# Optimization experiments

Measured on AMD Instinct MI355X. Metric: run time of the kernel, lower is better.

Reference implementation:

```python
import jax, jax.numpy as jnp
import numpy as np

# Model constants (from init_kwargs)
NF, NC, E, B = 100000, 4000, 500000, 256
D_FACT, D_COMP = 1536, 27
HIDDEN, HEADS, CPH = 128, 4, 32  # out_per_head = hidden // heads
NUM_LAYERS = 2
TIME_DIM = 8
T_SCALE = 30.0
EDGE_DIM = 2 + TIME_DIM  # [sentiment, decay, time2vec]
ATTN_SCALE = 1.0  # 1 / attn_temperature
NEG_SLOPE = 0.2


def time_edge_features(ea, lam):
    # ea: [E, 2] = [sentiment, decay]; second column in [0,1] -> decay branch
    s = jnp.clip(ea[:, 0:1], -1.0, 1.0)
    decay = jnp.clip(ea[:, 1:2], 0.0, 1.0)
    lam = jnp.maximum(lam, 1e-6)
    delta_t = -jnp.log(jnp.maximum(decay, 1e-6)) / lam
    t = jnp.log1p(jnp.maximum(delta_t, 0.0)) / T_SCALE  # [E,1]
    freqs = jnp.arange(1, TIME_DIM, dtype=ea.dtype)      # [TIME_DIM-1]
    sins = jnp.sin(t * freqs)                            # [E,TIME_DIM-1]
    return jnp.concatenate([s, decay, sins, t], axis=-1)  # [E, EDGE_DIM]


def seg_softmax(logits, seg, n):
    # logits: [E,H]; softmax over edges sharing the same destination node
    m = jax.ops.segment_max(logits, seg, num_segments=n)
    z = jnp.exp(logits - m[seg])
    den = jax.ops.segment_sum(z, seg, num_segments=n)
    return z / (den[seg] + 1e-16)


def seg_mean(x, seg, n):
    s = jax.ops.segment_sum(x, seg, num_segments=n)
    cnt = jax.ops.segment_sum(jnp.ones((x.shape[0],), x.dtype), seg, num_segments=n)
    return s / jnp.maximum(cnt, 1.0)[:, None]


def layernorm(x, g, b, eps=1e-5):
    mu = jnp.mean(x, axis=-1, keepdims=True)
    var = jnp.var(x, axis=-1, keepdims=True)
    return (x - mu) * jax.lax.rsqrt(var + eps) * g + b


def setup_inputs() -> dict:
    key = jax.random.key(0)
    ks = jax.random.split(key, 32)

    x_fact = jax.random.normal(ks[0], (NF, D_FACT), jnp.float32)
    x_company = jax.random.normal(ks[1], (NC, D_COMP), jnp.float32)
    u = jax.random.uniform(ks[2], (E, 2), jnp.float32)
    edge_attr = jnp.concatenate([u[:, 0:1] * 2.0 - 1.0, u[:, 1:2]], axis=1)
    edge_index = jnp.stack([
        jax.random.randint(ks[3], (E,), 0, NF),
        jax.random.randint(ks[4], (E,), 0, NC),
    ]).astype(jnp.int32)
    batch_fact = jnp.sort(jax.random.randint(ks[5], (NF,), 0, B)).astype(jnp.int32)
    batch_company = jnp.sort(jax.random.randint(ks[6], (NC,), 0, B)).astype(jnp.int32)

    def p(k, shape):
        return jax.random.normal(k, shape, jnp.float32) * 0.05

    inp = dict(
        x_fact=x_fact, x_company=x_company, edge_attr=edge_attr,
        edge_index=edge_index, batch_fact=batch_fact, batch_company=batch_company,
        lambda_decay=jnp.array(0.01, jnp.float32),
        Wf=p(ks[7], (D_FACT, HIDDEN)), bf=jnp.zeros((HIDDEN,), jnp.float32),
        Wc=p(ks[8], (D_COMP, HIDDEN)), bc=jnp.zeros((HIDDEN,), jnp.float32),
        Wl=p(ks[9], (NUM_LAYERS, HIDDEN, HIDDEN)), bl=jnp.zeros((NUM_LAYERS, HIDDEN), jnp.float32),
        Wr=p(ks[10], (NUM_LAYERS, HIDDEN, HIDDEN)), br=jnp.zeros((NUM_LAYERS, HIDDEN), jnp.float32),
        We=p(ks[11], (NUM_LAYERS, EDGE_DIM, HIDDEN)), be=jnp.zeros((NUM_LAYERS, HIDDEN), jnp.float32),
        att=p(ks[12], (NUM_LAYERS, HEADS, CPH)),
        bias_out=jnp.zeros((NUM_LAYERS, HIDDEN), jnp.float32),
        ln_g=jnp.ones((NUM_LAYERS, HIDDEN), jnp.float32), ln_b=jnp.zeros((NUM_LAYERS, HIDDEN), jnp.float32),
        Wg=p(ks[13], (2 * HIDDEN, 1)), bg=jnp.zeros((1,), jnp.float32),
        W1=p(ks[14], (HIDDEN, HIDDEN)), b1=jnp.zeros((HIDDEN,), jnp.float32),
        W2=p(ks[15], (HIDDEN, 1)), b2=jnp.zeros((1,), jnp.float32),
    )
    return inp


def reference(x_fact, x_company, edge_attr, edge_index, batch_fact, batch_company,
              lambda_decay, Wf, bf, Wc, bc, Wl, bl, Wr, br, We, be, att, bias_out,
              ln_g, ln_b, Wg, bg, W1, b1, W2, b2):
    src, dst = edge_index[0], edge_index[1]
    ef = time_edge_features(edge_attr, lambda_decay)          # [E, EDGE_DIM]

    # per-node-type input encoders
    hf = jax.nn.relu(x_fact @ Wf + bf)                         # [NF, H]
    hc = jax.nn.relu(x_company @ Wc + bc)                      # [NC, H]
    n_c = x_company.shape[0]

    for l in range(NUM_LAYERS):
        # GATv2 (edge-conditioned, bipartite fact->company, share_weights=False)
        gl = (hf @ Wl[l] + bl[l]).reshape(-1, HEADS, CPH)      # src transform [NF,H,C]
        gr = (hc @ Wr[l] + br[l]).reshape(-1, HEADS, CPH)      # dst transform [NC,H,C]
        ge = (ef @ We[l] + be[l]).reshape(-1, HEADS, CPH)      # edge transform [E,H,C]
        e = jax.nn.leaky_relu(gl[src] + gr[dst] + ge, NEG_SLOPE)  # [E,H,C]
        logits = jnp.einsum('ehc,hc->eh', e, att[l]) * ATTN_SCALE  # [E,H]
        alpha = seg_softmax(logits, dst, n_c)                   # scatter-softmax over dst
        msg = alpha[..., None] * gl[src]                        # [E,H,C]
        out = jax.ops.segment_sum(msg, dst, num_segments=n_c).reshape(n_c, HIDDEN) + bias_out[l]
        hc = layernorm(hc + jax.nn.relu(out), ln_g[l], ln_b[l])  # residual + post-norm

    # gated readout over graphs in batch
    pf = seg_mean(hf, batch_fact, B)                            # [B,H]
    pc = seg_mean(hc, batch_company, B)                         # [B,H]
    g = jax.nn.sigmoid(jnp.concatenate([pf, pc], axis=-1) @ Wg + bg)  # [B,1]
    h = g * pf + (1.0 - g) * pc                                 # [B,H]
    logit = jax.nn.relu(h @ W1 + b1) @ W2 + b2                  # [B,1]
    return logit
```

## Files before the change

kernel.cpp:

```cpp
#include <hip/hip_runtime.h>
#include <hip/hip_bf16.h>
#include <hip/hip_fp16.h>
#include <math.h>

#define NFAC 100000
#define NCOMP 4000
#define NEDGE 500000
#define NB 256
#define DF 1536
#define DC 27
#define H 128
#define EDIM 10
#define EDIMP 16

typedef __attribute__((ext_vector_type(8))) short short8v;
typedef __attribute__((ext_vector_type(4))) float f32x4;

#define GLOAD_LDS16(g, l)                                                              \
  __builtin_amdgcn_global_load_lds((const __attribute__((address_space(1))) unsigned int*)(g), \
                                   (__attribute__((address_space(3))) unsigned int*)(l), 16, 0, 0)

__device__ __forceinline__ float group32_sum(float v) {
#pragma unroll
  for (int m = 16; m > 0; m >>= 1) v += __shfl_xor(v, m);
  return v;
}

__device__ __forceinline__ unsigned short bf16rn(float x) {
  unsigned int u = __float_as_uint(x);
  unsigned int r = (u + 0x7fffu + ((u >> 16) & 1u)) >> 16;
  return (unsigned short)r;
}
__device__ __forceinline__ float bf16tof(unsigned short h) {
  return __uint_as_float(((unsigned int)h) << 16);
}

__global__ void k_edge_feat(const float* __restrict__ ea, const float* __restrict__ lamp,
                            float* __restrict__ ef) {
  int e = blockIdx.x * blockDim.x + threadIdx.x;
  if (e >= NEDGE) return;
  float s   = fminf(fmaxf(ea[2 * e], -1.f), 1.f);
  float dec = fminf(fmaxf(ea[2 * e + 1], 0.f), 1.f);
  float lam = fmaxf(lamp[0], 1e-6f);
  float dt  = -logf(fmaxf(dec, 1e-6f)) / lam;
  float t   = log1pf(fmaxf(dt, 0.f)) * (1.f / 30.f);
  float* o = ef + (size_t)e * EDIMP;
  o[0] = s;
  o[1] = dec;
#pragma unroll
  for (int k = 1; k < 8; k++) o[1 + k] = __sinf(t * (float)k);
  o[9] = t;
  o[10] = 0.f; o[11] = 0.f; o[12] = 0.f; o[13] = 0.f; o[14] = 0.f; o[15] = 0.f;
}

__global__ void k_hist(const int* __restrict__ dst, int* __restrict__ deg) {
  int e = blockIdx.x * blockDim.x + threadIdx.x;
  if (e < NEDGE) atomicAdd(&deg[dst[e]], 1);
}

__global__ __launch_bounds__(1024) void k_scan(const int* __restrict__ deg, int* __restrict__ off) {
  __shared__ int s[4096];
  int t = threadIdx.x;
  for (int i = t; i < 4096; i += 1024) s[i] = (i < NCOMP) ? deg[i] : 0;
  __syncthreads();
  for (int d = 1; d < 4096; d <<= 1) {
    int vals[4];
#pragma unroll
    for (int j = 0; j < 4; j++) {
      int i = t + j * 1024;
      vals[j] = (i >= d) ? s[i - d] : 0;
    }
    __syncthreads();
#pragma unroll
    for (int j = 0; j < 4; j++) {
      int i = t + j * 1024;
      s[i] += vals[j];
    }
    __syncthreads();
  }
  for (int i = t; i < 4096; i += 1024) off[i + 1] = s[i];
  if (t == 0) off[0] = 0;
}

__global__ void k_scatter(const int* __restrict__ dst, const int* __restrict__ src,
                          const int* __restrict__ off, int* __restrict__ cur,
                          int* __restrict__ eid, int* __restrict__ srcs) {
  int e = blockIdx.x * blockDim.x + threadIdx.x;
  if (e < NEDGE) {
    int d = dst[e];
    int p = atomicAdd(&cur[d], 1);
    eid[off[d] + p] = e;
    srcs[off[d] + p] = src[e];
  }
}

__global__ void k_conv_w(const float* __restrict__ W, unsigned short* __restrict__ Bh,
                         unsigned short* __restrict__ Bl, int K) {
  int i = blockIdx.x * blockDim.x + threadIdx.x;
  if (i >= K * H) return;
  int k = i >> 7, c = i & 127;
  float x = W[i];
  unsigned short h = bf16rn(x);
  unsigned short l = bf16rn(x - bf16tof(h));
  Bh[(size_t)c * K + k] = h;
  Bl[(size_t)c * K + k] = l;
}

__global__ void k_conv_wl2(const float* __restrict__ Wl, unsigned short* __restrict__ Bh,
                           unsigned short* __restrict__ Bl) {
  int i = blockIdx.x * blockDim.x + threadIdx.x;
  if (i >= 2 * H * H) return;
  int l = i >> 14;
  int r = i & 16383;
  int k = r >> 7, c = r & 127;
  float x = Wl[i];
  unsigned short h = bf16rn(x);
  unsigned short lo = bf16rn(x - bf16tof(h));
  int col = c + 128 * l;
  Bh[(size_t)col * H + k] = h;
  Bl[(size_t)col * H + k] = lo;
}

__device__ __forceinline__ unsigned int packhi(unsigned int u1, unsigned int u0) {
  return __builtin_amdgcn_perm(u1, u0, 0x07060302u);
}

__device__ __forceinline__ void split8(const float4& a0, const float4& a1, short8v& ah,
                                       short8v& al) {
  float xs[8] = {a0.x, a0.y, a0.z, a0.w, a1.x, a1.y, a1.z, a1.w};
  unsigned int hu[8], lu[8];
#pragma unroll
  for (int j = 0; j < 8; j++) {
    unsigned int u = __float_as_uint(xs[j]);
    hu[j] = u & 0xffff0000u;
    lu[j] = __float_as_uint(xs[j] - __uint_as_float(hu[j]));
  }
  unsigned int hw[4], lw[4];
#pragma unroll
  for (int j = 0; j < 4; j++) {
    hw[j] = packhi(hu[2 * j + 1], hu[2 * j]);
    lw[j] = packhi(lu[2 * j + 1], lu[2 * j]);
  }
  ah = *(short8v*)hw;
  al = *(short8v*)lw;
}

__global__ __launch_bounds__(256, 2) void k_gemm_mfma(const float* __restrict__ A,
                                                      const unsigned short* __restrict__ Bth,
                                                      const unsigned short* __restrict__ Btl,
                                                      const float* __restrict__ bias,
                                                      float* __restrict__ C, int M, int K,
                                                      int dorelu, float* __restrict__ Cpart) {
  __shared__ __align__(16) char smem[2][32768];
  int tid = threadIdx.x;
  int wave = tid >> 6, lane = tid & 63;
  int m0 = blockIdx.x * 128;
  int wm = (wave >> 1) * 64, wn = (wave & 1) * 64;
  int fr = lane & 15, fg = lane >> 4;
  int nsplit = gridDim.y;
  int Ks = K / nsplit;
  int kbeg = blockIdx.y * Ks;
  int nIter = Ks >> 5;

  f32x4 acc[4][4];
#pragma unroll
  for (int i = 0; i < 4; i++)
#pragma unroll
    for (int j = 0; j < 4; j++) acc[i][j] = (f32x4){0.f, 0.f, 0.f, 0.f};

  int a_row = (lane >> 3);
  int a_s = lane & 7;
  int b_col = (lane >> 2);
  int b_s = lane & 3;

  auto stage = [&](int buf, int k0) {
    char* base = smem[buf];
#pragma unroll
    for (int q = 0; q < 4; q++) {
      int j = wave + 4 * q;
      int row = j * 8 + a_row;
      int grow = m0 + row;
      if (grow >= M) grow = 0;
      const float* src = A + (size_t)grow * K + k0 + ((a_s ^ (row & 7)) << 2);
      GLOAD_LDS16(src, base + j * 1024);
    }
#pragma unroll
    for (int q = 0; q < 2; q++) {
      int j = wave + 4 * q;
      int col = j * 16 + b_col;
      int soff = k0 + ((b_s ^ (col & 3)) << 3);
      GLOAD_LDS16(Bth + (size_t)col * K + soff, base + 16384 + j * 1024);
      GLOAD_LDS16(Btl + (size_t)col * K + soff, base + 24576 + j * 1024);
    }
  };

  stage(0, kbeg);
  __syncthreads();

  for (int it = 0; it < nIter; ++it) {
    int cur = it & 1;
    if (it + 1 < nIter) stage(cur ^ 1, kbeg + ((it + 1) << 5));
    const char* cb = smem[cur];
    short8v ah[4], al[4];
#pragma unroll
    for (int mf = 0; mf < 4; mf++) {
      int r = wm + 16 * mf + fr;
      int s0 = (2 * fg) ^ (r & 7);
      int s1 = (2 * fg + 1) ^ (r & 7);
      float4 a0 = *(const float4*)(cb + r * 128 + s0 * 16);
      float4 a1 = *(const float4*)(cb + r * 128 + s1 * 16);
      split8(a0, a1, ah[mf], al[mf]);
    }
#pragma unroll
    for (int nf = 0; nf < 4; nf++) {
      int c = wn + 16 * nf + fr;
      int sb = fg ^ (c & 3);
      short8v bh = *(const short8v*)(cb + 16384 + c * 64 + sb * 16);
      short8v bl = *(const short8v*)(cb + 24576 + c * 64 + sb * 16);
#pragma unroll
      for (int mf = 0; mf < 4; mf++) {
        acc[mf][nf] = __builtin_amdgcn_mfma_f32_16x16x32_bf16(ah[mf], bh, acc[mf][nf], 0, 0, 0);
        acc[mf][nf] = __builtin_amdgcn_mfma_f32_16x16x32_bf16(ah[mf], bl, acc[mf][nf], 0, 0, 0);
        acc[mf][nf] = __builtin_amdgcn_mfma_f32_16x16x32_bf16(al[mf], bh, acc[mf][nf], 0, 0, 0);
      }
    }
    __syncthreads();
  }

  if (nsplit == 1) {
#pragma unroll
    for (int mf = 0; mf < 4; mf++) {
      int rbase = m0 + wm + 16 * mf + 4 * fg;
#pragma unroll
      for (int nf = 0; nf < 4; nf++) {
        int col = wn + 16 * nf + fr;
        float bv = bias[col];
#pragma unroll
        for (int j = 0; j < 4; j++) {
          int row = rbase + j;
          if (row < M) {
            float v = acc[mf][nf][j] + bv;
            if (dorelu) v = fmaxf(v, 0.f);
            C[(size_t)row * H + col] = v;
          }
        }
      }
    }
  } else {
    float* P = Cpart + (size_t)blockIdx.y * M * H;
#pragma unroll
    for (int mf = 0; mf < 4; mf++) {
      int rbase = m0 + wm + 16 * mf + 4 * fg;
#pragma unroll
      for (int nf = 0; nf < 4; nf++) {
        int col = wn + 16 * nf + fr;
#pragma unroll
        for (int j = 0; j < 4; j++) {
          int row = rbase + j;
          if (row < M) P[(size_t)row * H + col] = acc[mf][nf][j];
        }
      }
    }
  }
}

__global__ __launch_bounds__(256, 2) void k_gemm_n256(const float* __restrict__ A,
                                                      const unsigned short* __restrict__ Bth,
                                                      const unsigned short* __restrict__ Btl,
                                                      const float* __restrict__ bias,
                                                      __half* __restrict__ C, int M) {
  __shared__ __align__(16) char smem[2][40960];
  const int K = 128;
  int tid = threadIdx.x;
  int wave = tid >> 6, lane = tid & 63;
  int m0 = blockIdx.x * 64;
  int wn = wave * 64;
  int fr = lane & 15, fg = lane >> 4;

  f32x4 acc[4][4];
#pragma unroll
  for (int i = 0; i < 4; i++)
#pragma unroll
    for (int j = 0; j < 4; j++) acc[i][j] = (f32x4){0.f, 0.f, 0.f, 0.f};

  int a_row = (lane >> 3);
  int a_s = lane & 7;
  int b_col = (lane >> 2);
  int b_s = lane & 3;

  auto stage = [&](int buf, int k0) {
    char* base = smem[buf];
#pragma unroll
    for (int q = 0; q < 2; q++) {
      int j = wave + 4 * q;
      int row = j * 8 + a_row;
      int grow = m0 + row;
      if (grow >= M) grow = 0;
      GLOAD_LDS16(A + (size_t)grow * K + k0 + ((a_s ^ (row & 7)) << 2), base + j * 1024);
    }
#pragma unroll
    for (int q = 0; q < 4; q++) {
      int j = wave + 4 * q;
      int col = j * 16 + b_col;
      int soff = k0 + ((b_s ^ (col & 3)) << 3);
      GLOAD_LDS16(Bth + (size_t)col * K + soff, base + 8192 + j * 1024);
      GLOAD_LDS16(Btl + (size_t)col * K + soff, base + 24576 + j * 1024);
    }
  };

  stage(0, 0);
  __syncthreads();

  for (int it = 0; it < 4; ++it) {
    int cur = it & 1;
    if (it + 1 < 4) stage(cur ^ 1, (it + 1) << 5);
    const char* cb = smem[cur];
    short8v ah[4], al[4];
#pragma unroll
    for (int mf = 0; mf < 4; mf++) {
      int r = 16 * mf + fr;
      int s0 = (2 * fg) ^ (r & 7);
      int s1 = (2 * fg + 1) ^ (r & 7);
      float4 a0 = *(const float4*)(cb + r * 128 + s0 * 16);
      float4 a1 = *(const float4*)(cb + r * 128 + s1 * 16);
      split8(a0, a1, ah[mf], al[mf]);
    }
#pragma unroll
    for (int nf = 0; nf < 4; nf++) {
      int c = wn + 16 * nf + fr;
      int sb = fg ^ (c & 3);
      short8v bh = *(const short8v*)(cb + 8192 + c * 64 + sb * 16);
      short8v bl = *(const short8v*)(cb + 24576 + c * 64 + sb * 16);
#pragma unroll
      for (int mf = 0; mf < 4; mf++) {
        acc[mf][nf] = __builtin_amdgcn_mfma_f32_16x16x32_bf16(ah[mf], bh, acc[mf][nf], 0, 0, 0);
        acc[mf][nf] = __builtin_amdgcn_mfma_f32_16x16x32_bf16(ah[mf], bl, acc[mf][nf], 0, 0, 0);
        acc[mf][nf] = __builtin_amdgcn_mfma_f32_16x16x32_bf16(al[mf], bh, acc[mf][nf], 0, 0, 0);
      }
    }
    __syncthreads();
  }

#pragma unroll
  for (int mf = 0; mf < 4; mf++) {
    int rbase = m0 + 16 * mf + 4 * fg;
#pragma unroll
    for (int nf = 0; nf < 4; nf++) {
      int col = wn + 16 * nf + fr;
      float bv = bias[col];
#pragma unroll
      for (int j = 0; j < 4; j++) {
        int row = rbase + j;
        if (row < M) C[(size_t)row * 256 + col] = __float2half(acc[mf][nf][j] + bv);
      }
    }
  }
}

__global__ __launch_bounds__(256) void k_reduce2(const float* __restrict__ P0,
                                                 const float* __restrict__ P1,
                                                 const float* __restrict__ bias,
                                                 float* __restrict__ C, int total4) {
  int i = blockIdx.x * blockDim.x + threadIdx.x;
  if (i >= total4) return;
  float4 a = ((const float4*)P0)[i];
  float4 b = ((const float4*)P1)[i];
  float4 bv = ((const float4*)bias)[i & 31];
  float4 r;
  r.x = fmaxf(a.x + b.x + bv.x, 0.f);
  r.y = fmaxf(a.y + b.y + bv.y, 0.f);
  r.z = fmaxf(a.z + b.z + bv.z, 0.f);
  r.w = fmaxf(a.w + b.w + bv.w, 0.f);
  ((float4*)C)[i] = r;
}

__global__ void k_enc_comp(const float* __restrict__ X, const float* __restrict__ Wc,
                           const float* __restrict__ bc, float* __restrict__ hc) {
  int tid = threadIdx.x;
  int r = blockIdx.x * 2 + (tid >> 7);
  int j = tid & 127;
  if (r >= NCOMP) return;
  float acc = bc[j];
  const float* x = X + (size_t)r * DC;
#pragma unroll
  for (int k = 0; k < DC; k++) acc = fmaf(x[k], Wc[k * H + j], acc);
  hc[(size_t)r * H + j] = fmaxf(acc, 0.f);
}

__global__ __launch_bounds__(128) void k_node(
    const __half* __restrict__ gl, const float* __restrict__ ef, const int* __restrict__ srcs,
    const int* __restrict__ csr_off, const int* __restrict__ csr_eid,
    const float* __restrict__ Wr, const float* __restrict__ br, const float* __restrict__ We,
    const float* __restrict__ be, const float* __restrict__ att,
    const float* __restrict__ bias_out, const float* __restrict__ lng,
    const float* __restrict__ lnb, float* __restrict__ hc) {
  int v = blockIdx.x;
  int t = threadIdx.x;
  __shared__ float hcs[H];
  __shared__ float red[2], redq[2];
  float x = hc[(size_t)v * H + t];
  hcs[t] = x;
  float wre[EDIM];
#pragma unroll
  for (int k = 0; k < EDIM; k++) wre[k] = We[k * H + t];
  float attv = att[t];
  float bev = be[t];
  __syncthreads();
  float grv = br[t];
  for (int k = 0; k < H; k++) grv = fmaf(hcs[k], Wr[k * H + t], grv);
  float grb = grv + bev;

  int e0 = csr_off[v], e1 = csr_off[v + 1];
  float m = -INFINITY, s = 0.f, acc = 0.f;
  int i = e0;
  int eid = 0, sid = 0;
  if (i < e1) {
    eid = csr_eid[i];
    sid = srcs[i];
  }
  while (i < e1) {
    float glv = __half2float(gl[(size_t)sid * 256 + t]);
    const float* efr = ef + (size_t)eid * EDIMP;
    float4 f0 = *(const float4*)(efr);
    float4 f1 = *(const float4*)(efr + 4);
    float2 f2 = *(const float2*)(efr + 8);
    int ni = i + 1;
    if (ni < e1) {
      eid = csr_eid[ni];
      sid = srcs[ni];
    }
    float ge = grb;
    ge = fmaf(f0.x, wre[0], ge);
    ge = fmaf(f0.y, wre[1], ge);
    ge = fmaf(f0.z, wre[2], ge);
    ge = fmaf(f0.w, wre[3], ge);
    ge = fmaf(f1.x, wre[4], ge);
    ge = fmaf(f1.y, wre[5], ge);
    ge = fmaf(f1.z, wre[6], ge);
    ge = fmaf(f1.w, wre[7], ge);
    ge = fmaf(f2.x, wre[8], ge);
    ge = fmaf(f2.y, wre[9], ge);
    float ev = glv + ge;
    ev = ev > 0.f ? ev : 0.2f * ev;
    float logit = group32_sum(ev * attv);
    if (logit > m) {
      float scale = __expf(m - logit);
      s = s * scale + 1.f;
      acc = acc * scale + glv;
      m = logit;
    } else {
      float z = __expf(logit - m);
      s += z;
      acc = fmaf(z, glv, acc);
    }
    i = ni;
  }
  float outv = acc / (s + 1e-16f);
  outv += bias_out[t];
  outv = fmaxf(outv, 0.f);
  float y = x + outv;
  float sv = y, qv = y * y;
#pragma unroll
  for (int mm = 32; mm > 0; mm >>= 1) {
    sv += __shfl_xor(sv, mm);
    qv += __shfl_xor(qv, mm);
  }
  int wid = t >> 6, lane = t & 63;
  if (lane == 0) {
    red[wid] = sv;
    redq[wid] = qv;
  }
  __syncthreads();
  float mean = (red[0] + red[1]) * (1.f / H);
  float var = (redq[0] + redq[1]) * (1.f / H) - mean * mean;
  float r = rsqrtf(var + 1e-5f);
  hc[(size_t)v * H + t] = (y - mean) * r * lng[t] + lnb[t];
}

template <int CHUNK>
__global__ __launch_bounds__(128) void k_segmean(const float* __restrict__ X,
                                                 const int* __restrict__ seg, int n,
                                                 float* __restrict__ sum, int* __restrict__ cnt) {
  int t = threadIdx.x;
  int n0 = blockIdx.x * CHUNK;
  int n1 = min(n0 + CHUNK, n);
  float acc = 0.f;
  int c = 0;
  int curs = -1;
  for (int i = n0; i < n1; ++i) {
    int sg = seg[i];
    if (sg != curs) {
      if (curs >= 0) {
        atomicAdd(&sum[(size_t)curs * H + t], acc);
        if (t == 0) atomicAdd(&cnt[curs], c);
      }
      curs = sg;
      acc = 0.f;
      c = 0;
    }
    acc += X[(size_t)i * H + t];
    c++;
  }
  if (curs >= 0) {
    atomicAdd(&sum[(size_t)curs * H + t], acc);
    if (t == 0) atomicAdd(&cnt[curs], c);
  }
}

__global__ __launch_bounds__(128) void k_readout(const float* __restrict__ pf,
                                                 const float* __restrict__ pc,
                                                 const int* __restrict__ cf,
                                                 const int* __restrict__ cc,
                                                 const float* __restrict__ Wg,
                                                 const float* __restrict__ bg,
                                                 const float* __restrict__ W1,
                                                 const float* __restrict__ b1,
                                                 const float* __restrict__ W2,
                                                 const float* __restrict__ b2,
                                                 float* __restrict__ out) {
  int b = blockIdx.x, t = threadIdx.x;
  __shared__ float hs[H];
  __shared__ float red[2], red2[2];
  int wid = t >> 6, lane = t & 63;
  float nf = fmaxf((float)cf[b], 1.f);
  float nc = fmaxf((float)cc[b], 1.f);
  float pfv = pf[(size_t)b * H + t] / nf;
  float pcv = pc[(size_t)b * H + t] / nc;
  float gp = pfv * Wg[t] + pcv * Wg[H + t];
  float sv = gp;
#pragma unroll
  for (int mm = 32; mm > 0; mm >>= 1) sv += __shfl_xor(sv, mm);
  if (lane == 0) red[wid] = sv;
  __syncthreads();
  float g = 1.f / (1.f + expf(-(red[0] + red[1] + bg[0])));
  float h = g * pfv + (1.f - g) * pcv;
  hs[t] = h;
  __syncthreads();
  float a = b1[t];
  for (int k = 0; k < H; k++) a = fmaf(hs[k], W1[k * H + t], a);
  a = fmaxf(a, 0.f);
  float p = a * W2[t];
#pragma unroll
  for (int mm = 32; mm > 0; mm >>= 1) p += __shfl_xor(p, mm);
  if (lane == 0) red2[wid] = p;
  __syncthreads();
  if (t == 0) out[b] = red2[0] + red2[1] + b2[0];
}

extern "C" void kernel_launch(void* const* d_in, const int* in_sizes, int n_in, void* d_out,
                              int out_size, void* d_ws, size_t ws_size, hipStream_t stream) {
  const float* x_fact = (const float*)d_in[0];
  const float* x_comp = (const float*)d_in[1];
  const float* ea = (const float*)d_in[2];
  const int* eidx = (const int*)d_in[3];
  const int* batf = (const int*)d_in[4];
  const int* batc = (const int*)d_in[5];
  const float* lam = (const float*)d_in[6];
  const float* Wf = (const float*)d_in[7];
  const float* bf = (const float*)d_in[8];
  const float* Wc = (const float*)d_in[9];
  const float* bc = (const float*)d_in[10];
  const float* Wl = (const float*)d_in[11];
  const float* bl = (const float*)d_in[12];
  const float* Wr = (const float*)d_in[13];
  const float* br_ = (const float*)d_in[14];
  const float* We = (const float*)d_in[15];
  const float* be = (const float*)d_in[16];
  const float* att = (const float*)d_in[17];
  const float* b_out = (const float*)d_in[18];
  const float* lng = (const float*)d_in[19];
  const float* lnb = (const float*)d_in[20];
  const float* Wg = (const float*)d_in[21];
  const float* bg = (const float*)d_in[22];
  const float* W1 = (const float*)d_in[23];
  const float* b1 = (const float*)d_in[24];
  const float* W2 = (const float*)d_in[25];
  const float* b2 = (const float*)d_in[26];
  float* out = (float*)d_out;

  char* w = (char*)d_ws;
  auto carve = [&](size_t bytes) -> char* {
    char* p = w;
    w += (bytes + 255) & ~(size_t)255;
    return p;
  };
  float* HF = (float*)carve((size_t)NFAC * H * 4);
  float* GL = (float*)carve((size_t)NFAC * H * 4);
  float* CP1 = (float*)carve((size_t)NFAC * H * 4);
  __half* GL2 = (__half*)GL;
  float* HC = (float*)carve((size_t)NCOMP * H * 4);
  float* EF = (float*)carve((size_t)NEDGE * EDIMP * 4);
  int* OFF = (int*)carve(4100 * 4);
  int* EID = (int*)carve((size_t)NEDGE * 4);
  int* SRCS = (int*)carve((size_t)NEDGE * 4);
  unsigned short* WfH = (unsigned short*)carve((size_t)DF * H * 2);
  unsigned short* WfL = (unsigned short*)carve((size_t)DF * H * 2);
  unsigned short* WlH2 = (unsigned short*)carve((size_t)256 * H * 2);
  unsigned short* WlL2 = (unsigned short*)carve((size_t)256 * H * 2);
  char* zbase = w;
  int* DEG = (int*)carve(4096 * 4);
  int* CUR = (int*)carve(4096 * 4);
  float* PF = (float*)carve((size_t)NB * H * 4);
  float* PC = (float*)carve((size_t)NB * H * 4);
  int* CF = (int*)carve(NB * 4);
  int* CC = (int*)carve(NB * 4);
  size_t zbytes = (size_t)(w - zbase);
  hipMemsetAsync(zbase, 0, zbytes, stream);

  const int* srcArr = eidx;
  const int* dstArr = eidx + NEDGE;

  k_edge_feat<<<(NEDGE + 255) / 256, 256, 0, stream>>>(ea, lam, EF);
  k_hist<<<(NEDGE + 255) / 256, 256, 0, stream>>>(dstArr, DEG);
  k_scan<<<1, 1024, 0, stream>>>(DEG, OFF);
  k_scatter<<<(NEDGE + 255) / 256, 256, 0, stream>>>(dstArr, srcArr, OFF, CUR, EID, SRCS);

  k_conv_w<<<(DF * H + 255) / 256, 256, 0, stream>>>(Wf, WfH, WfL, DF);
  k_conv_wl2<<<(2 * H * H + 255) / 256, 256, 0, stream>>>(Wl, WlH2, WlL2);

  {
    float* CPART = GL;
    dim3 grid((NFAC + 127) / 128, 2);
    k_gemm_mfma<<<grid, 256, 0, stream>>>(x_fact, WfH, WfL, bf, HF, NFAC, DF, 1, CPART);
    int total4 = NFAC * H / 4;
    k_reduce2<<<(total4 + 255) / 256, 256, 0, stream>>>(GL, CP1, bf, HF, total4);
  }
  k_enc_comp<<<NCOMP / 2, 256, 0, stream>>>(x_comp, Wc, bc, HC);

  k_gemm_n256<<<(NFAC + 63) / 64, 256, 0, stream>>>(HF, WlH2, WlL2, bl, GL2, NFAC);

  for (int l = 0; l < 2; l++) {
    k_node<<<NCOMP, 128, 0, stream>>>(GL2 + l * 128, EF, SRCS, OFF, EID,
                                      Wr + (size_t)l * H * H, br_ + l * H,
                                      We + (size_t)l * EDIM * H, be + l * H, att + l * H,
                                      b_out + l * H, lng + l * H, lnb + l * H, HC);
  }

  k_segmean<128><<<(NFAC + 127) / 128, 128, 0, stream>>>(HF, batf, NFAC, PF, CF);
  k_segmean<64><<<(NCOMP + 63) / 64, 128, 0, stream>>>(HC, batc, NCOMP, PC, CC);
  k_readout<<<NB, 128, 0, stream>>>(PF, PC, CF, CC, Wg, bg, W1, b1, W2, b2, out);
}
```

Baseline: 692.4 us.

## Load GEMM B fragments directly from global and dual-stream edge softmax

Both MFMA GEMM kernels stop staging the split-bf16 weight tiles through LDS. Each lane now loads its B fragments straight from global memory into registers, which shrinks shared memory per block and removes LDS traffic, but the B loads are no longer double-buffered ahead of use. The per-company attention kernel processes edges two at a time with independent online-softmax states that are merged at the end. This raises memory-level parallelism and removes the data-dependent branch, at the cost of extra exp calls.

```diff
diff --git a/kernel.cpp b/kernel.cpp
--- a/kernel.cpp
+++ b/kernel.cpp
@@ -151,7 +151,7 @@
                                                       const float* __restrict__ bias,
                                                       float* __restrict__ C, int M, int K,
                                                       int dorelu, float* __restrict__ Cpart) {
-  __shared__ __align__(16) char smem[2][32768];
+  __shared__ __align__(16) char smem[2][16384];
   int tid = threadIdx.x;
   int wave = tid >> 6, lane = tid & 63;
   int m0 = blockIdx.x * 128;
@@ -170,10 +170,17 @@
 
   int a_row = (lane >> 3);
   int a_s = lane & 7;
-  int b_col = (lane >> 2);
-  int b_s = lane & 3;
-
-  auto stage = [&](int buf, int k0) {
+
+  const unsigned short* bhp[4];
+  const unsigned short* blp[4];
+#pragma unroll
+  for (int nf = 0; nf < 4; nf++) {
+    int col = wn + 16 * nf + fr;
+    bhp[nf] = Bth + (size_t)col * K + kbeg + fg * 8;
+    blp[nf] = Btl + (size_t)col * K + kbeg + fg * 8;
+  }
+
+  auto stageA = [&](int buf, int k0) {
     char* base = smem[buf];
 #pragma unroll
     for (int q = 0; q < 4; q++) {
@@ -184,22 +191,21 @@
       const float* src = A + (size_t)grow * K + k0 + ((a_s ^ (row & 7)) << 2);
       GLOAD_LDS16(src, base + j * 1024);
     }
-#pragma unroll
-    for (int q = 0; q < 2; q++) {
-      int j = wave + 4 * q;
-      int col = j * 16 + b_col;
-      int soff = k0 + ((b_s ^ (col & 3)) << 3);
-      GLOAD_LDS16(Bth + (size_t)col * K + soff, base + 16384 + j * 1024);
-      GLOAD_LDS16(Btl + (size_t)col * K + soff, base + 24576 + j * 1024);
-    }
   };
 
-  stage(0, kbeg);
+  stageA(0, kbeg);
   __syncthreads();
 
   for (int it = 0; it < nIter; ++it) {
     int cur = it & 1;
-    if (it + 1 < nIter) stage(cur ^ 1, kbeg + ((it + 1) << 5));
+    int k0 = it << 5;
+    short8v bh[4], bl[4];
+#pragma unroll
+    for (int nf = 0; nf < 4; nf++) {
+      bh[nf] = *(const short8v*)(bhp[nf] + k0);
+      bl[nf] = *(const short8v*)(blp[nf] + k0);
+    }
+    if (it + 1 < nIter) stageA(cur ^ 1, kbeg + ((it + 1) << 5));
     const char* cb = smem[cur];
     short8v ah[4], al[4];
 #pragma unroll
@@ -213,15 +219,11 @@
     }
 #pragma unroll
     for (int nf = 0; nf < 4; nf++) {
-      int c = wn + 16 * nf + fr;
-      int sb = fg ^ (c & 3);
-      short8v bh = *(const short8v*)(cb + 16384 + c * 64 + sb * 16);
-      short8v bl = *(const short8v*)(cb + 24576 + c * 64 + sb * 16);
 #pragma unroll
       for (int mf = 0; mf < 4; mf++) {
-        acc[mf][nf] = __builtin_amdgcn_mfma_f32_16x16x32_bf16(ah[mf], bh, acc[mf][nf], 0, 0, 0);
-        acc[mf][nf] = __builtin_amdgcn_mfma_f32_16x16x32_bf16(ah[mf], bl, acc[mf][nf], 0, 0, 0);
-        acc[mf][nf] = __builtin_amdgcn_mfma_f32_16x16x32_bf16(al[mf], bh, acc[mf][nf], 0, 0, 0);
+        acc[mf][nf] = __builtin_amdgcn_mfma_f32_16x16x32_bf16(ah[mf], bh[nf], acc[mf][nf], 0, 0, 0);
+        acc[mf][nf] = __builtin_amdgcn_mfma_f32_16x16x32_bf16(ah[mf], bl[nf], acc[mf][nf], 0, 0, 0);
+        acc[mf][nf] = __builtin_amdgcn_mfma_f32_16x16x32_bf16(al[mf], bh[nf], acc[mf][nf], 0, 0, 0);
       }
     }
     __syncthreads();
@@ -269,7 +271,7 @@
                                                       const unsigned short* __restrict__ Btl,
                                                       const float* __restrict__ bias,
                                                       __half* __restrict__ C, int M) {
-  __shared__ __align__(16) char smem[2][40960];
+  __shared__ __align__(16) char smem[2][8192];
   const int K = 128;
   int tid = threadIdx.x;
   int wave = tid >> 6, lane = tid & 63;
@@ -285,10 +287,17 @@
 
   int a_row = (lane >> 3);
   int a_s = lane & 7;
-  int b_col = (lane >> 2);
-  int b_s = lane & 3;
-
-  auto stage = [&](int buf, int k0) {
+
+  const unsigned short* bhp[4];
+  const unsigned short* blp[4];
+#pragma unroll
+  for (int nf = 0; nf < 4; nf++) {
+    int col = wn + 16 * nf + fr;
+    bhp[nf] = Bth + (size_t)col * K + fg * 8;
+    blp[nf] = Btl + (size_t)col * K + fg * 8;
+  }
+
+  auto stageA = [&](int buf, int k0) {
     char* base = smem[buf];
 #pragma unroll
     for (int q = 0; q < 2; q++) {
@@ -298,22 +307,21 @@
       if (grow >= M) grow = 0;
       GLOAD_LDS16(A + (size_t)grow * K + k0 + ((a_s ^ (row & 7)) << 2), base + j * 1024);
     }
-#pragma unroll
-    for (int q = 0; q < 4; q++) {
-      int j = wave + 4 * q;
-      int col = j * 16 + b_col;
-      int soff = k0 + ((b_s ^ (col & 3)) << 3);
-      GLOAD_LDS16(Bth + (size_t)col * K + soff, base + 8192 + j * 1024);
-      GLOAD_LDS16(Btl + (size_t)col * K + soff, base + 24576 + j * 1024);
-    }
   };
 
-  stage(0, 0);
+  stageA(0, 0);
   __syncthreads();
 
   for (int it = 0; it < 4; ++it) {
     int cur = it & 1;
-    if (it + 1 < 4) stage(cur ^ 1, (it + 1) << 5);
+    int k0 = it << 5;
+    short8v bh[4], bl[4];
+#pragma unroll
+    for (int nf = 0; nf < 4; nf++) {
+      bh[nf] = *(const short8v*)(bhp[nf] + k0);
+      bl[nf] = *(const short8v*)(blp[nf] + k0);
+    }
+    if (it + 1 < 4) stageA(cur ^ 1, (it + 1) << 5);
     const char* cb = smem[cur];
     short8v ah[4], al[4];
 #pragma unroll
@@ -327,15 +335,11 @@
     }
 #pragma unroll
     for (int nf = 0; nf < 4; nf++) {
-      int c = wn + 16 * nf + fr;
-      int sb = fg ^ (c & 3);
-      short8v bh = *(const short8v*)(cb + 8192 + c * 64 + sb * 16);
-      short8v bl = *(const short8v*)(cb + 24576 + c * 64 + sb * 16);
 #pragma unroll
       for (int mf = 0; mf < 4; mf++) {
-        acc[mf][nf] = __builtin_amdgcn_mfma_f32_16x16x32_bf16(ah[mf], bh, acc[mf][nf], 0, 0, 0);
-        acc[mf][nf] = __builtin_amdgcn_mfma_f32_16x16x32_bf16(ah[mf], bl, acc[mf][nf], 0, 0, 0);
-        acc[mf][nf] = __builtin_amdgcn_mfma_f32_16x16x32_bf16(al[mf], bh, acc[mf][nf], 0, 0, 0);
+        acc[mf][nf] = __builtin_amdgcn_mfma_f32_16x16x32_bf16(ah[mf], bh[nf], acc[mf][nf], 0, 0, 0);
+        acc[mf][nf] = __builtin_amdgcn_mfma_f32_16x16x32_bf16(ah[mf], bl[nf], acc[mf][nf], 0, 0, 0);
+        acc[mf][nf] = __builtin_amdgcn_mfma_f32_16x16x32_bf16(al[mf], bh[nf], acc[mf][nf], 0, 0, 0);
       }
     }
     __syncthreads();
@@ -411,59 +415,100 @@
   float grb = grv + bev;
 
   int e0 = csr_off[v], e1 = csr_off[v + 1];
-  float m = -INFINITY, s = 0.f, acc = 0.f;
+  float mA = -INFINITY, sA = 0.f, aA = 0.f;
+  float mB = -INFINITY, sB = 0.f, aB = 0.f;
   int i = e0;
-  int eid = 0, sid = 0;
+  while (i + 1 < e1) {
+    int eA = csr_eid[i], sdA = srcs[i];
+    int eB = csr_eid[i + 1], sdB = srcs[i + 1];
+    float glA = __half2float(gl[(size_t)sdA * 256 + t]);
+    float glB = __half2float(gl[(size_t)sdB * 256 + t]);
+    const float* fA = ef + (size_t)eA * EDIMP;
+    const float* fB = ef + (size_t)eB * EDIMP;
+    float4 a0 = *(const float4*)(fA);
+    float4 a1 = *(const float4*)(fA + 4);
+    float2 a2 = *(const float2*)(fA + 8);
+    float4 b0 = *(const float4*)(fB);
+    float4 b1 = *(const float4*)(fB + 4);
+    float2 b2 = *(const float2*)(fB + 8);
+    float geA = grb, geB = grb;
+    geA = fmaf(a0.x, wre[0], geA); geB = fmaf(b0.x, wre[0], geB);
+    geA = fmaf(a0.y, wre[1], geA); geB = fmaf(b0.y, wre[1], geB);
+    geA = fmaf(a0.z, wre[2], geA); geB = fmaf(b0.z, wre[2], geB);
+    geA = fmaf(a0.w, wre[3], geA); geB = fmaf(b0.w, wre[3], geB);
+    geA = fmaf(a1.x, wre[4], geA); geB = fmaf(b1.x, wre[4], geB);
+    geA = fmaf(a1.y, wre[5], geA); geB = fmaf(b1.y, wre[5], geB);
+    geA = fmaf(a1.z, wre[6], geA); geB = fmaf(b1.z, wre[6], geB);
+    geA = fmaf(a1.w, wre[7], geA); geB = fmaf(b1.w, wre[7], geB);
+    geA = fmaf(a2.x, wre[8], geA); geB = fmaf(b2.x, wre[8], geB);
+    geA = fmaf(a2.y, wre[9], geA); geB = fmaf(b2.y, wre[9], geB);
+    float evA = glA + geA;
+    float evB = glB + geB;
+    evA = evA > 0.f ? evA : 0.2f * evA;
+    evB = evB > 0.f ? evB : 0.2f * evB;
+    float lA = evA * attv, lB = evB * attv;
+#pragma unroll
+    for (int mm = 16; mm > 0; mm >>= 1) {
+      lA += __shfl_xor(lA, mm);
+      lB += __shfl_xor(lB, mm);
+    }
+    float mnA = fmaxf(mA, lA);
+    float scA = __expf(mA - mnA);
+    float zA = __expf(lA - mnA);
+    sA = fmaf(sA, scA, zA);
+    aA = fmaf(aA, scA, zA * glA);
+    mA = mnA;
+    float mnB = fmaxf(mB, lB);
+    float scB = __expf(mB - mnB);
+    float zB = __expf(lB - mnB);
+    sB = fmaf(sB, scB, zB);
+    aB = fmaf(aB, scB, zB * glB);
+    mB = mnB;
+    i += 2;
+  }
   if (i < e1) {
-    eid = csr_eid[i];
-    sid = srcs[i];
-  }
-  while (i < e1) {
-    float glv = __half2float(gl[(size_t)sid * 256 + t]);
-    const float* efr = ef + (size_t)eid * EDIMP;
-    float4 f0 = *(const float4*)(efr);
-    float4 f1 = *(const float4*)(efr + 4);
-    float2 f2 = *(const float2*)(efr + 8);
-    int ni = i + 1;
-    if (ni < e1) {
-      eid = csr_eid[ni];
-      sid = srcs[ni];
-    }
-    float ge = grb;
-    ge = fmaf(f0.x, wre[0], ge);
-    ge = fmaf(f0.y, wre[1], ge);
-    ge = fmaf(f0.z, wre[2], ge);
-    ge = fmaf(f0.w, wre[3], ge);
-    ge = fmaf(f1.x, wre[4], ge);
-    ge = fmaf(f1.y, wre[5], ge);
-    ge = fmaf(f1.z, wre[6], ge);
-    ge = fmaf(f1.w, wre[7], ge);
-    ge = fmaf(f2.x, wre[8], ge);
-    ge = fmaf(f2.y, wre[9], ge);
-    float ev = glv + ge;
-    ev = ev > 0.f ? ev : 0.2f * ev;
-    float logit = group32_sum(ev * attv);
-    if (logit > m) {
-      float scale = __expf(m - logit);
-      s = s * scale + 1.f;
-      acc = acc * scale + glv;
-      m = logit;
-    } else {
-      float z = __expf(logit - m);
-      s += z;
-      acc = fmaf(z, glv, acc);
-    }
-    i = ni;
-  }
+    int eA = csr_eid[i], sdA = srcs[i];
+    float glA = __half2float(gl[(size_t)sdA * 256 + t]);
+    const float* fA = ef + (size_t)eA * EDIMP;
+    float4 a0 = *(const float4*)(fA);
+    float4 a1 = *(const float4*)(fA + 4);
+    float2 a2 = *(const float2*)(fA + 8);
+    float geA = grb;
+    geA = fmaf(a0.x, wre[0], geA);
+    geA = fmaf(a0.y, wre[1], geA);
+    geA = fmaf(a0.z, wre[2], geA);
+    geA = fmaf(a0.w, wre[3], geA);
+    geA = fmaf(a1.x, wre[4], geA);
+    geA = fmaf(a1.y, wre[5], geA);
+    geA = fmaf(a1.z, wre[6], geA);
+    geA = fmaf(a1.w, wre[7], geA);
+    geA = fmaf(a2.x, wre[8], geA);
+    geA = fmaf(a2.y, wre[9], geA);
+    float evA = glA + geA;
+    evA = evA > 0.f ? evA : 0.2f * evA;
+    float lA = group32_sum(evA * attv);
+    float mnA = fmaxf(mA, lA);
+    float scA = __expf(mA - mnA);
+    float zA = __expf(lA - mnA);
+    sA = fmaf(sA, scA, zA);
+    aA = fmaf(aA, scA, zA * glA);
+    mA = mnA;
+  }
+  float mm = fmaxf(mA, mB);
+  float wAc = (mA > -INFINITY) ? __expf(mA - mm) : 0.f;
+  float wBc = (mB > -INFINITY) ? __expf(mB - mm) : 0.f;
+  float s = sA * wAc + sB * wBc;
+  float acc = aA * wAc + aB * wBc;
+
   float outv = acc / (s + 1e-16f);
   outv += bias_out[t];
   outv = fmaxf(outv, 0.f);
   float y = x + outv;
   float sv = y, qv = y * y;
 #pragma unroll
-  for (int mm = 32; mm > 0; mm >>= 1) {
-    sv += __shfl_xor(sv, mm);
-    qv += __shfl_xor(qv, mm);
+  for (int mm2 = 32; mm2 > 0; mm2 >>= 1) {
+    sv += __shfl_xor(sv, mm2);
+    qv += __shfl_xor(qv, mm2);
   }
   int wid = t >> 6, lane = t & 63;
   if (lane == 0) {
```

Result: no change. 695.8 us (+0.5%).

## Load GEMM B fragments directly from global, drop split-K, fuse node layers

Applied to the files above, without the earlier changes.

Both MFMA GEMMs now read the bf16 hi/lo weight fragments straight from global memory into registers instead of staging them through LDS. This cuts shared memory per block and may raise occupancy. The fact-encoder GEMM drops its two-way split-K and the separate reduce kernel, writing bias plus ReLU directly. The two per-layer k_node launches are merged into one kernel that loops over both layers, keeping the company state in shared memory between them. The trade-offs are fewer blocks for the large GEMM, and repeated uncached-pattern global reads of B per wave.

```diff
diff --git a/kernel.cpp b/kernel.cpp
--- a/kernel.cpp
+++ b/kernel.cpp
@@ -150,17 +150,14 @@
                                                       const unsigned short* __restrict__ Btl,
                                                       const float* __restrict__ bias,
                                                       float* __restrict__ C, int M, int K,
-                                                      int dorelu, float* __restrict__ Cpart) {
-  __shared__ __align__(16) char smem[2][32768];
+                                                      int dorelu) {
+  __shared__ __align__(16) char smem[2][16384];
   int tid = threadIdx.x;
   int wave = tid >> 6, lane = tid & 63;
   int m0 = blockIdx.x * 128;
   int wm = (wave >> 1) * 64, wn = (wave & 1) * 64;
   int fr = lane & 15, fg = lane >> 4;
-  int nsplit = gridDim.y;
-  int Ks = K / nsplit;
-  int kbeg = blockIdx.y * Ks;
-  int nIter = Ks >> 5;
+  int nIter = K >> 5;
 
   f32x4 acc[4][4];
 #pragma unroll
@@ -170,10 +167,17 @@
 
   int a_row = (lane >> 3);
   int a_s = lane & 7;
-  int b_col = (lane >> 2);
-  int b_s = lane & 3;
-
-  auto stage = [&](int buf, int k0) {
+
+  const unsigned short* bhp[4];
+  const unsigned short* blp[4];
+#pragma unroll
+  for (int nf = 0; nf < 4; nf++) {
+    int col = wn + 16 * nf + fr;
+    bhp[nf] = Bth + (size_t)col * K + fg * 8;
+    blp[nf] = Btl + (size_t)col * K + fg * 8;
+  }
+
+  auto stageA = [&](int buf, int k0) {
     char* base = smem[buf];
 #pragma unroll
     for (int q = 0; q < 4; q++) {
@@ -184,22 +188,21 @@
       const float* src = A + (size_t)grow * K + k0 + ((a_s ^ (row & 7)) << 2);
       GLOAD_LDS16(src, base + j * 1024);
     }
-#pragma unroll
-    for (int q = 0; q < 2; q++) {
-      int j = wave + 4 * q;
-      int col = j * 16 + b_col;
-      int soff = k0 + ((b_s ^ (col & 3)) << 3);
-      GLOAD_LDS16(Bth + (size_t)col * K + soff, base + 16384 + j * 1024);
-      GLOAD_LDS16(Btl + (size_t)col * K + soff, base + 24576 + j * 1024);
-    }
   };
 
-  stage(0, kbeg);
+  stageA(0, 0);
   __syncthreads();
 
   for (int it = 0; it < nIter; ++it) {
     int cur = it & 1;
-    if (it + 1 < nIter) stage(cur ^ 1, kbeg + ((it + 1) << 5));
+    int k0 = it << 5;
+    short8v bh[4], bl[4];
+#pragma unroll
+    for (int nf = 0; nf < 4; nf++) {
+      bh[nf] = *(const short8v*)(bhp[nf] + k0);
+      bl[nf] = *(const short8v*)(blp[nf] + k0);
+    }
+    if (it + 1 < nIter) stageA(cur ^ 1, (it + 1) << 5);
     const char* cb = smem[cur];
     short8v ah[4], al[4];
 #pragma unroll
@@ -213,51 +216,30 @@
     }
 #pragma unroll
     for (int nf = 0; nf < 4; nf++) {
-      int c = wn + 16 * nf + fr;
-      int sb = fg ^ (c & 3);
-      short8v bh = *(const short8v*)(cb + 16384 + c * 64 + sb * 16);
-      short8v bl = *(const short8v*)(cb + 24576 + c * 64 + sb * 16);
 #pragma unroll
       for (int mf = 0; mf < 4; mf++) {
-        acc[mf][nf] = __builtin_amdgcn_mfma_f32_16x16x32_bf16(ah[mf], bh, acc[mf][nf], 0, 0, 0);
-        acc[mf][nf] = __builtin_amdgcn_mfma_f32_16x16x32_bf16(ah[mf], bl, acc[mf][nf], 0, 0, 0);
-        acc[mf][nf] = __builtin_amdgcn_mfma_f32_16x16x32_bf16(al[mf], bh, acc[mf][nf], 0, 0, 0);
+        acc[mf][nf] = __builtin_amdgcn_mfma_f32_16x16x32_bf16(ah[mf], bh[nf], acc[mf][nf], 0, 0, 0);
+        acc[mf][nf] = __builtin_amdgcn_mfma_f32_16x16x32_bf16(ah[mf], bl[nf], acc[mf][nf], 0, 0, 0);
+        acc[mf][nf] = __builtin_amdgcn_mfma_f32_16x16x32_bf16(al[mf], bh[nf], acc[mf][nf], 0, 0, 0);
       }
     }
     __syncthreads();
   }
 
-  if (nsplit == 1) {
-#pragma unroll
-    for (int mf = 0; mf < 4; mf++) {
-      int rbase = m0 + wm + 16 * mf + 4 * fg;
-#pragma unroll
-      for (int nf = 0; nf < 4; nf++) {
-        int col = wn + 16 * nf + fr;
-        float bv = bias[col];
-#pragma unroll
-        for (int j = 0; j < 4; j++) {
-          int row = rbase + j;
-          if (row < M) {
-            float v = acc[mf][nf][j] + bv;
-            if (dorelu) v = fmaxf(v, 0.f);
-            C[(size_t)row * H + col] = v;
-          }
-        }
-      }
-    }
-  } else {
-    float* P = Cpart + (size_t)blockIdx.y * M * H;
-#pragma unroll
-    for (int mf = 0; mf < 4; mf++) {
-      int rbase = m0 + wm + 16 * mf + 4 * fg;
-#pragma unroll
-      for (int nf = 0; nf < 4; nf++) {
-        int col = wn + 16 * nf + fr;
-#pragma unroll
-        for (int j = 0; j < 4; j++) {
-          int row = rbase + j;
-          if (row < M) P[(size_t)row * H + col] = acc[mf][nf][j];
+#pragma unroll
+  for (int mf = 0; mf < 4; mf++) {
+    int rbase = m0 + wm + 16 * mf + 4 * fg;
+#pragma unroll
+    for (int nf = 0; nf < 4; nf++) {
+      int col = wn + 16 * nf + fr;
+      float bv = bias[col];
+#pragma unroll
+      for (int j = 0; j < 4; j++) {
+        int row = rbase + j;
+        if (row < M) {
+          float v = acc[mf][nf][j] + bv;
+          if (dorelu) v = fmaxf(v, 0.f);
+          C[(size_t)row * H + col] = v;
         }
       }
     }
@@ -269,7 +251,7 @@
                                                       const unsigned short* __restrict__ Btl,
                                                       const float* __restrict__ bias,
                                                       __half* __restrict__ C, int M) {
-  __shared__ __align__(16) char smem[2][40960];
+  __shared__ __align__(16) char smem[2][8192];
   const int K = 128;
   int tid = threadIdx.x;
   int wave = tid >> 6, lane = tid & 63;
@@ -285,10 +267,17 @@
 
   int a_row = (lane >> 3);
   int a_s = lane & 7;
-  int b_col = (lane >> 2);
-  int b_s = lane & 3;
-
-  auto stage = [&](int buf, int k0) {
+
+  const unsigned short* bhp[4];
+  const unsigned short* blp[4];
+#pragma unroll
+  for (int nf = 0; nf < 4; nf++) {
+    int col = wn + 16 * nf + fr;
+    bhp[nf] = Bth + (size_t)col * K + fg * 8;
+    blp[nf] = Btl + (size_t)col * K + fg * 8;
+  }
+
+  auto stageA = [&](int buf, int k0) {
     char* base = smem[buf];
 #pragma unroll
     for (int q = 0; q < 2; q++) {
@@ -298,22 +287,21 @@
       if (grow >= M) grow = 0;
       GLOAD_LDS16(A + (size_t)grow * K + k0 + ((a_s ^ (row & 7)) << 2), base + j * 1024);
     }
-#pragma unroll
-    for (int q = 0; q < 4; q++) {
-      int j = wave + 4 * q;
-      int col = j * 16 + b_col;
-      int soff = k0 + ((b_s ^ (col & 3)) << 3);
-      GLOAD_LDS16(Bth + (size_t)col * K + soff, base + 8192 + j * 1024);
-      GLOAD_LDS16(Btl + (size_t)col * K + soff, base + 24576 + j * 1024);
-    }
   };
 
-  stage(0, 0);
+  stageA(0, 0);
   __syncthreads();
 
   for (int it = 0; it < 4; ++it) {
     int cur = it & 1;
-    if (it + 1 < 4) stage(cur ^ 1, (it + 1) << 5);
+    int k0 = it << 5;
+    short8v bh[4], bl[4];
+#pragma unroll
+    for (int nf = 0; nf < 4; nf++) {
+      bh[nf] = *(const short8v*)(bhp[nf] + k0);
+      bl[nf] = *(const short8v*)(blp[nf] + k0);
+    }
+    if (it + 1 < 4) stageA(cur ^ 1, (it + 1) << 5);
     const char* cb = smem[cur];
     short8v ah[4], al[4];
 #pragma unroll
@@ -327,15 +315,11 @@
     }
 #pragma unroll
     for (int nf = 0; nf < 4; nf++) {
-      int c = wn + 16 * nf + fr;
-      int sb = fg ^ (c & 3);
-      short8v bh = *(const short8v*)(cb + 8192 + c * 64 + sb * 16);
-      short8v bl = *(const short8v*)(cb + 24576 + c * 64 + sb * 16);
 #pragma unroll
       for (int mf = 0; mf < 4; mf++) {
-        acc[mf][nf] = __builtin_amdgcn_mfma_f32_16x16x32_bf16(ah[mf], bh, acc[mf][nf], 0, 0, 0);
-        acc[mf][nf] = __builtin_amdgcn_mfma_f32_16x16x32_bf16(ah[mf], bl, acc[mf][nf], 0, 0, 0);
-        acc[mf][nf] = __builtin_amdgcn_mfma_f32_16x16x32_bf16(al[mf], bh, acc[mf][nf], 0, 0, 0);
+        acc[mf][nf] = __builtin_amdgcn_mfma_f32_16x16x32_bf16(ah[mf], bh[nf], acc[mf][nf], 0, 0, 0);
+        acc[mf][nf] = __builtin_amdgcn_mfma_f32_16x16x32_bf16(ah[mf], bl[nf], acc[mf][nf], 0, 0, 0);
+        acc[mf][nf] = __builtin_amdgcn_mfma_f32_16x16x32_bf16(al[mf], bh[nf], acc[mf][nf], 0, 0, 0);
       }
     }
     __syncthreads();
@@ -355,23 +339,6 @@
       }
     }
   }
-}
-
-__global__ __launch_bounds__(256) void k_reduce2(const float* __restrict__ P0,
-                                                 const float* __restrict__ P1,
-                                                 const float* __restrict__ bias,
-                                                 float* __restrict__ C, int total4) {
-  int i = blockIdx.x * blockDim.x + threadIdx.x;
-  if (i >= total4) return;
-  float4 a = ((const float4*)P0)[i];
-  float4 b = ((const float4*)P1)[i];
-  float4 bv = ((const float4*)bias)[i & 31];
-  float4 r;
-  r.x = fmaxf(a.x + b.x + bv.x, 0.f);
-  r.y = fmaxf(a.y + b.y + bv.y, 0.f);
-  r.z = fmaxf(a.z + b.z + bv.z, 0.f);
-  r.w = fmaxf(a.w + b.w + bv.w, 0.f);
-  ((float4*)C)[i] = r;
 }
 
 __global__ void k_enc_comp(const float* __restrict__ X, const float* __restrict__ Wc,
@@ -387,8 +354,8 @@
   hc[(size_t)r * H + j] = fmaxf(acc, 0.f);
 }
 
-__global__ __launch_bounds__(128) void k_node(
-    const __half* __restrict__ gl, const float* __restrict__ ef, const int* __restrict__ srcs,
+__global__ __launch_bounds__(128) void k_node2(
+    const __half* __restrict__ gl2, const float* __restrict__ ef, const int* __restrict__ srcs,
     const int* __restrict__ csr_off, const int* __restrict__ csr_eid,
     const float* __restrict__ Wr, const float* __restrict__ br, const float* __restrict__ We,
     const float* __restrict__ be, const float* __restrict__ att,
@@ -400,81 +367,92 @@
   __shared__ float red[2], redq[2];
   float x = hc[(size_t)v * H + t];
   hcs[t] = x;
-  float wre[EDIM];
-#pragma unroll
-  for (int k = 0; k < EDIM; k++) wre[k] = We[k * H + t];
-  float attv = att[t];
-  float bev = be[t];
+  int e0 = csr_off[v], e1 = csr_off[v + 1];
   __syncthreads();
-  float grv = br[t];
-  for (int k = 0; k < H; k++) grv = fmaf(hcs[k], Wr[k * H + t], grv);
-  float grb = grv + bev;
-
-  int e0 = csr_off[v], e1 = csr_off[v + 1];
-  float m = -INFINITY, s = 0.f, acc = 0.f;
-  int i = e0;
-  int eid = 0, sid = 0;
-  if (i < e1) {
-    eid = csr_eid[i];
-    sid = srcs[i];
-  }
-  while (i < e1) {
-    float glv = __half2float(gl[(size_t)sid * 256 + t]);
-    const float* efr = ef + (size_t)eid * EDIMP;
-    float4 f0 = *(const float4*)(efr);
-    float4 f1 = *(const float4*)(efr + 4);
-    float2 f2 = *(const float2*)(efr + 8);
-    int ni = i + 1;
-    if (ni < e1) {
-      eid = csr_eid[ni];
-      sid = srcs[ni];
-    }
-    float ge = grb;
-    ge = fmaf(f0.x, wre[0], ge);
-    ge = fmaf(f0.y, wre[1], ge);
-    ge = fmaf(f0.z, wre[2], ge);
-    ge = fmaf(f0.w, wre[3], ge);
-    ge = fmaf(f1.x, wre[4], ge);
-    ge = fmaf(f1.y, wre[5], ge);
-    ge = fmaf(f1.z, wre[6], ge);
-    ge = fmaf(f1.w, wre[7], ge);
-    ge = fmaf(f2.x, wre[8], ge);
-    ge = fmaf(f2.y, wre[9], ge);
-    float ev = glv + ge;
-    ev = ev > 0.f ? ev : 0.2f * ev;
-    float logit = group32_sum(ev * attv);
-    if (logit > m) {
-      float scale = __expf(m - logit);
-      s = s * scale + 1.f;
-      acc = acc * scale + glv;
-      m = logit;
-    } else {
-      float z = __expf(logit - m);
-      s += z;
-      acc = fmaf(z, glv, acc);
-    }
-    i = ni;
-  }
-  float outv = acc / (s + 1e-16f);
-  outv += bias_out[t];
-  outv = fmaxf(outv, 0.f);
-  float y = x + outv;
-  float sv = y, qv = y * y;
-#pragma unroll
-  for (int mm = 32; mm > 0; mm >>= 1) {
-    sv += __shfl_xor(sv, mm);
-    qv += __shfl_xor(qv, mm);
-  }
-  int wid = t >> 6, lane = t & 63;
-  if (lane == 0) {
-    red[wid] = sv;
-    redq[wid] = qv;
-  }
-  __syncthreads();
-  float mean = (red[0] + red[1]) * (1.f / H);
-  float var = (redq[0] + redq[1]) * (1.f / H) - mean * mean;
-  float r = rsqrtf(var + 1e-5f);
-  hc[(size_t)v * H + t] = (y - mean) * r * lng[t] + lnb[t];
+
+  float y = x;
+#pragma unroll 1
+  for (int l = 0; l < 2; l++) {
+    const float* Wrl = Wr + (size_t)l * H * H;
+    float wre[EDIM];
+#pragma unroll
+    for (int k = 0; k < EDIM; k++) wre[k] = We[l * EDIM * H + k * H + t];
+    float attv = att[l * H + t];
+    float bev = be[l * H + t];
+    float grv = br[l * H + t];
+    for (int k = 0; k < H; k++) grv = fmaf(hcs[k], Wrl[k * H + t], grv);
+    float grb = grv + bev;
+    const __half* gl = gl2 + l * 128;
+
+    float m = -INFINITY, s = 0.f, acc = 0.f;
+    int i = e0;
+    int eid = 0, sid = 0;
+    if (i < e1) {
+      eid = csr_eid[i];
+      sid = srcs[i];
+    }
+    while (i < e1) {
+      float glv = __half2float(gl[(size_t)sid * 256 + t]);
+      const float* efr = ef + (size_t)eid * EDIMP;
+      float4 f0 = *(const float4*)(efr);
+      float4 f1 = *(const float4*)(efr + 4);
+      float2 f2 = *(const float2*)(efr + 8);
+      int ni = i + 1;
+      if (ni < e1) {
+        eid = csr_eid[ni];
+        sid = srcs[ni];
+      }
+      float ge = grb;
+      ge = fmaf(f0.x, wre[0], ge);
+      ge = fmaf(f0.y, wre[1], ge);
+      ge = fmaf(f0.z, wre[2], ge);
+      ge = fmaf(f0.w, wre[3], ge);
+      ge = fmaf(f1.x, wre[4], ge);
+      ge = fmaf(f1.y, wre[5], ge);
+      ge = fmaf(f1.z, wre[6], ge);
+      ge = fmaf(f1.w, wre[7], ge);
+      ge = fmaf(f2.x, wre[8], ge);
+      ge = fmaf(f2.y, wre[9], ge);
+      float ev = glv + ge;
+      ev = ev > 0.f ? ev : 0.2f * ev;
+      float logit = group32_sum(ev * attv);
+      if (logit > m) {
+        float scale = __expf(m - logit);
+        s = s * scale + 1.f;
+        acc = acc * scale + glv;
+        m = logit;
+      } else {
+        float z = __expf(logit - m);
+        s += z;
+        acc = fmaf(z, glv, acc);
+      }
+      i = ni;
+    }
+    float outv = acc / (s + 1e-16f);
+    outv += bias_out[l * H + t];
+    outv = fmaxf(outv, 0.f);
+    y = x + outv;
+    float sv = y, qv = y * y;
+#pragma unroll
+    for (int mm = 32; mm > 0; mm >>= 1) {
+      sv += __shfl_xor(sv, mm);
+      qv += __shfl_xor(qv, mm);
+    }
+    int wid = t >> 6, lane = t & 63;
+    if (lane == 0) {
+      red[wid] = sv;
+      redq[wid] = qv;
+    }
+    __syncthreads();
+    float mean = (red[0] + red[1]) * (1.f / H);
+    float var = (redq[0] + redq[1]) * (1.f / H) - mean * mean;
+    float r = rsqrtf(var + 1e-5f);
+    y = (y - mean) * r * lng[l * H + t] + lnb[l * H + t];
+    hcs[t] = y;
+    x = y;
+    __syncthreads();
+  }
+  hc[(size_t)v * H + t] = y;
 }
 
 template <int CHUNK>
@@ -585,9 +563,7 @@
     return p;
   };
   float* HF = (float*)carve((size_t)NFAC * H * 4);
-  float* GL = (float*)carve((size_t)NFAC * H * 4);
-  float* CP1 = (float*)carve((size_t)NFAC * H * 4);
-  __half* GL2 = (__half*)GL;
+  __half* GL2 = (__half*)carve((size_t)NFAC * 256 * 2);
   float* HC = (float*)carve((size_t)NCOMP * H * 4);
   float* EF = (float*)carve((size_t)NEDGE * EDIMP * 4);
   int* OFF = (int*)carve(4100 * 4);
@@ -618,23 +594,13 @@
   k_conv_w<<<(DF * H + 255) / 256, 256, 0, stream>>>(Wf, WfH, WfL, DF);
   k_conv_wl2<<<(2 * H * H + 255) / 256, 256, 0, stream>>>(Wl, WlH2, WlL2);
 
-  {
-    float* CPART = GL;
-    dim3 grid((NFAC + 127) / 128, 2);
-    k_gemm_mfma<<<grid, 256, 0, stream>>>(x_fact, WfH, WfL, bf, HF, NFAC, DF, 1, CPART);
-    int total4 = NFAC * H / 4;
-    k_reduce2<<<(total4 + 255) / 256, 256, 0, stream>>>(GL, CP1, bf, HF, total4);
-  }
+  k_gemm_mfma<<<(NFAC + 127) / 128, 256, 0, stream>>>(x_fact, WfH, WfL, bf, HF, NFAC, DF, 1);
   k_enc_comp<<<NCOMP / 2, 256, 0, stream>>>(x_comp, Wc, bc, HC);
 
   k_gemm_n256<<<(NFAC + 63) / 64, 256, 0, stream>>>(HF, WlH2, WlL2, bl, GL2, NFAC);
 
-  for (int l = 0; l < 2; l++) {
-    k_node<<<NCOMP, 128, 0, stream>>>(GL2 + l * 128, EF, SRCS, OFF, EID,
-                                      Wr + (size_t)l * H * H, br_ + l * H,
-                                      We + (size_t)l * EDIM * H, be + l * H, att + l * H,
-                                      b_out + l * H, lng + l * H, lnb + l * H, HC);
-  }
+  k_node2<<<NCOMP, 128, 0, stream>>>(GL2, EF, SRCS, OFF, EID, Wr, br_, We, be, att, b_out, lng,
+                                     lnb, HC);
 
   k_segmean<128><<<(NFAC + 127) / 128, 128, 0, stream>>>(HF, batf, NFAC, PF, CF);
   k_segmean<64><<<(NCOMP + 63) / 64, 128, 0, stream>>>(HC, batc, NCOMP, PC, CC);
```

Result: slower. 814.5 us (+17.6%).
